# Kernel tuning notes

Measured on AMD Instinct MI355X. Metric: run time of the kernel, lower is better.

## Reference

```python
import jax, jax.numpy as jnp
import numpy as np

HIDDEN = 2048
NUM_HEADS = 32
NUM_KV_HEADS = 8
HEAD_DIM = HIDDEN // NUM_HEADS  # 64


def setup_inputs() -> dict:
    key = jax.random.key(0)
    ks = jax.random.split(key, 5)
    s = 0.02
    x = jax.random.normal(ks[0], (2, 2048, HIDDEN), dtype=jnp.float32)
    Wq = jax.random.normal(ks[1], (HIDDEN, NUM_HEADS * HEAD_DIM), dtype=jnp.float32) * s
    Wk = jax.random.normal(ks[2], (HIDDEN, NUM_KV_HEADS * HEAD_DIM), dtype=jnp.float32) * s
    Wv = jax.random.normal(ks[3], (HIDDEN, NUM_KV_HEADS * HEAD_DIM), dtype=jnp.float32) * s
    Wo = jax.random.normal(ks[4], (NUM_HEADS * HEAD_DIM, HIDDEN), dtype=jnp.float32) * s
    return {"x": x, "Wq": Wq, "Wk": Wk, "Wv": Wv, "Wo": Wo}


def reference(x, Wq, Wk, Wv, Wo):
    b, s, _ = x.shape
    # projections: [b, s, h, d] -> [b, h, s, d]
    q = (x @ Wq).reshape(b, s, NUM_HEADS, HEAD_DIM).transpose(0, 2, 1, 3)
    k = (x @ Wk).reshape(b, s, NUM_KV_HEADS, HEAD_DIM).transpose(0, 2, 1, 3)
    v = (x @ Wv).reshape(b, s, NUM_KV_HEADS, HEAD_DIM).transpose(0, 2, 1, 3)
    rep = NUM_HEADS // NUM_KV_HEADS
    # repeat_interleave along head dim (consecutive copies), matching torch
    k = jnp.repeat(k, rep, axis=1)
    v = jnp.repeat(v, rep, axis=1)
    scale = HEAD_DIM ** (-0.5)
    attn = jnp.einsum("bhqd,bhkd->bhqk", q, k) * scale  # [b,h,s,s]
    attn = jax.nn.softmax(attn, axis=-1)
    out = jnp.einsum("bhqk,bhkd->bhqd", attn, v)
    out = out.transpose(0, 2, 1, 3).reshape(b, s, NUM_HEADS * HEAD_DIM)
    return out @ Wo
```

## Files before the change

### kernel.cpp

```cpp
#include <hip/hip_runtime.h>

typedef __attribute__((ext_vector_type(8))) short short8;
typedef __attribute__((ext_vector_type(4))) float f32x4;
typedef __attribute__((ext_vector_type(4))) unsigned short u16x4;
typedef __attribute__((ext_vector_type(8))) unsigned short u16x8;

__device__ __forceinline__ unsigned short f2bf(float f) {
  union { float f; unsigned u; } v; v.f = f;
  unsigned r = v.u + 0x7FFFu + ((v.u >> 16) & 1u);
  return (unsigned short)(r >> 16);
}

#define GLL16(g, l) \
  __builtin_amdgcn_global_load_lds((const __attribute__((address_space(1))) void*)(g), \
                                   (__attribute__((address_space(3))) void*)(l), 16, 0, 0)

__device__ __forceinline__ void tpose_body(const float* __restrict__ in,
                                           unsigned short* __restrict__ out,
                                           int C, int ldo, int c0, int r0,
                                           float (*tile)[33], int tx, int ty) {
#pragma unroll
  for (int i = 0; i < 4; ++i)
    tile[ty + i * 8][tx] = in[(size_t)(r0 + ty + i * 8) * C + c0 + tx];
  __syncthreads();
#pragma unroll
  for (int i = 0; i < 4; ++i)
    out[(size_t)(c0 + ty + i * 8) * ldo + r0 + tx] = f2bf(tile[tx][ty + i * 8]);
}

__global__ __launch_bounds__(256) void prep_kernel(const float* __restrict__ x,
                                                   const float* __restrict__ Wq,
                                                   const float* __restrict__ Wk,
                                                   const float* __restrict__ Wv,
                                                   const float* __restrict__ Wo,
                                                   unsigned short* __restrict__ xb,
                                                   unsigned short* __restrict__ wqkvt,
                                                   unsigned short* __restrict__ wot) {
  __shared__ float tile[32][33];
  const int bid = blockIdx.x;
  if (bid < 4096) {
    const int i = bid * 256 + threadIdx.x;
    const f32x4* p = (const f32x4*)x;
    f32x4 a = p[2 * i], b = p[2 * i + 1];
    u16x8 r;
    r[0] = f2bf(a[0]); r[1] = f2bf(a[1]); r[2] = f2bf(a[2]); r[3] = f2bf(a[3]);
    r[4] = f2bf(b[0]); r[5] = f2bf(b[1]); r[6] = f2bf(b[2]); r[7] = f2bf(b[3]);
    ((u16x8*)xb)[i] = r;
    return;
  }
  const int tx = threadIdx.x & 31, ty = threadIdx.x >> 5;
  int b2 = bid - 4096;
  if (b2 < 4096) {
    tpose_body(Wq, wqkvt, 2048, 2048, (b2 & 63) * 32, (b2 >> 6) * 32, tile, tx, ty);
    return;
  }
  b2 -= 4096;
  if (b2 < 1024) {
    tpose_body(Wk, wqkvt + (size_t)2048 * 2048, 512, 2048, (b2 & 15) * 32, (b2 >> 4) * 32, tile, tx, ty);
    return;
  }
  b2 -= 1024;
  if (b2 < 1024) {
    tpose_body(Wv, wqkvt + (size_t)2560 * 2048, 512, 2048, (b2 & 15) * 32, (b2 >> 4) * 32, tile, tx, ty);
    return;
  }
  b2 -= 1024;
  tpose_body(Wo, wot, 2048, 2048, (b2 & 63) * 32, (b2 >> 6) * 32, tile, tx, ty);
}

__global__ __launch_bounds__(256) void gemm_qkv_kernel(const unsigned short* __restrict__ A,
                                                       const unsigned short* __restrict__ BT,
                                                       unsigned short* __restrict__ Cq,
                                                       unsigned short* __restrict__ VT) {
  __shared__ unsigned short As[2][128 * 32];
  __shared__ unsigned short Bs[2][128 * 32];
  const int tid = threadIdx.x;
  const int wave = tid >> 6, lane = tid & 63;
  const int r16 = lane & 15, g = lane >> 4;
  const int n0 = blockIdx.x * 128, m0 = blockIdx.y * 128;
  const int wr = wave >> 1, wc = wave & 1;
  f32x4 acc[4][4] = {};
  const int so = wave * 1024 + lane * 16;

  auto STAGE = [&](int kt, int bufi) {
    const int k0 = kt * 32;
#pragma unroll
    for (int i = 0; i < 2; ++i) {
      const int o = i * 4096 + so;
      const int row = o >> 6;
      const int ke = (o & 63) >> 1;
      GLL16(A + (size_t)(m0 + row) * 2048 + k0 + ke, (char*)As[bufi] + i * 4096 + wave * 1024);
      GLL16(BT + (size_t)(n0 + row) * 2048 + k0 + ke, (char*)Bs[bufi] + i * 4096 + wave * 1024);
    }
  };
  STAGE(0, 0);
  __syncthreads();
  for (int kt = 0; kt < 64; ++kt) {
    const int cur = kt & 1;
    if (kt < 63) STAGE(kt + 1, cur ^ 1);
    short8 af[4], bfr[4];
#pragma unroll
    for (int mi = 0; mi < 4; ++mi) {
      const int row = wr * 64 + mi * 16 + r16;
      af[mi] = *(const short8*)((const char*)As[cur] + row * 64 + g * 16);
    }
#pragma unroll
    for (int ni = 0; ni < 4; ++ni) {
      const int row = wc * 64 + ni * 16 + r16;
      bfr[ni] = *(const short8*)((const char*)Bs[cur] + row * 64 + g * 16);
    }
#pragma unroll
    for (int mi = 0; mi < 4; ++mi)
#pragma unroll
      for (int ni = 0; ni < 4; ++ni)
        acc[mi][ni] = __builtin_amdgcn_mfma_f32_16x16x32_bf16(af[mi], bfr[ni], acc[mi][ni], 0, 0, 0);
    __syncthreads();
  }
  const float qs = 0.18033688f;
#pragma unroll
  for (int mi = 0; mi < 4; ++mi) {
#pragma unroll
    for (int ni = 0; ni < 4; ++ni) {
      const int n = n0 + wc * 64 + ni * 16 + r16;
      const int mb = m0 + wr * 64 + mi * 16 + g * 4;
      f32x4 v = acc[mi][ni];
      if (n < 2560) {
        const float s = (n < 2048) ? qs : 1.0f;
#pragma unroll
        for (int r = 0; r < 4; ++r) Cq[(size_t)(mb + r) * 3072 + n] = f2bf(v[r] * s);
      } else {
        const int d = n - 2560;
        const int bb = mb >> 11, s0 = mb & 2047;
        const int s0p = (s0 & ~31) | (((s0 >> 2) & 3) << 3) | (((s0 >> 4) & 1) << 2);
        u16x4 pk;
#pragma unroll
        for (int r = 0; r < 4; ++r) pk[r] = f2bf(v[r]);
        *(u16x4*)(VT + (size_t)(bb * 512 + d) * 2048 + s0p) = pk;
      }
    }
  }
}

__global__ __launch_bounds__(256) void gemm_out_kernel(const unsigned short* __restrict__ A,
                                                       const unsigned short* __restrict__ BT,
                                                       float* __restrict__ Co) {
  __shared__ unsigned short As[2][128 * 32];
  __shared__ unsigned short Bs[2][128 * 32];
  const int tid = threadIdx.x;
  const int wave = tid >> 6, lane = tid & 63;
  const int r16 = lane & 15, g = lane >> 4;
  const int n0 = blockIdx.x * 128, m0 = blockIdx.y * 128;
  const int wr = wave >> 1, wc = wave & 1;
  f32x4 acc[4][4] = {};
  const int so = wave * 1024 + lane * 16;

  auto STAGE = [&](int kt, int bufi) {
    const int k0 = kt * 32;
#pragma unroll
    for (int i = 0; i < 2; ++i) {
      const int o = i * 4096 + so;
      const int row = o >> 6;
      const int ke = (o & 63) >> 1;
      GLL16(A + (size_t)(m0 + row) * 2048 + k0 + ke, (char*)As[bufi] + i * 4096 + wave * 1024);
      GLL16(BT + (size_t)(n0 + row) * 2048 + k0 + ke, (char*)Bs[bufi] + i * 4096 + wave * 1024);
    }
  };
  STAGE(0, 0);
  __syncthreads();
  for (int kt = 0; kt < 64; ++kt) {
    const int cur = kt & 1;
    if (kt < 63) STAGE(kt + 1, cur ^ 1);
    short8 af[4], bfr[4];
#pragma unroll
    for (int mi = 0; mi < 4; ++mi) {
      const int row = wr * 64 + mi * 16 + r16;
      af[mi] = *(const short8*)((const char*)As[cur] + row * 64 + g * 16);
    }
#pragma unroll
    for (int ni = 0; ni < 4; ++ni) {
      const int row = wc * 64 + ni * 16 + r16;
      bfr[ni] = *(const short8*)((const char*)Bs[cur] + row * 64 + g * 16);
    }
#pragma unroll
    for (int mi = 0; mi < 4; ++mi)
#pragma unroll
      for (int ni = 0; ni < 4; ++ni)
        acc[mi][ni] = __builtin_amdgcn_mfma_f32_16x16x32_bf16(af[mi], bfr[ni], acc[mi][ni], 0, 0, 0);
    __syncthreads();
  }
#pragma unroll
  for (int mi = 0; mi < 4; ++mi)
#pragma unroll
    for (int ni = 0; ni < 4; ++ni) {
      const int n = n0 + wc * 64 + ni * 16 + r16;
      const int mb = m0 + wr * 64 + mi * 16 + g * 4;
      f32x4 v = acc[mi][ni];
#pragma unroll
      for (int r = 0; r < 4; ++r) Co[(size_t)(mb + r) * 2048 + n] = v[r];
    }
}

__global__ __launch_bounds__(512) void attn_kernel(const unsigned short* __restrict__ QKV,
                                                   const unsigned short* __restrict__ VT,
                                                   unsigned short* __restrict__ O) {
  __shared__ unsigned short Ks[2][64 * 64];
  __shared__ unsigned short Vs[2][64 * 64];
  const int tid = threadIdx.x;
  const int wave = tid >> 6, lane = tid & 63;
  const int r16 = lane & 15, g = lane >> 4;
  const int qt = blockIdx.x, bh = blockIdx.y;
  const int b = bh >> 5, h = bh & 31, kvh = h >> 2;
  const int qtok0 = b * 2048 + qt * 128 + wave * 16;
  short8 qf[2];
#pragma unroll
  for (int kh = 0; kh < 2; ++kh)
    qf[kh] = *(const short8*)(QKV + (size_t)(qtok0 + r16) * 3072 + h * 64 + kh * 32 + g * 8);
  union { unsigned u[4]; short8 s; } ones;
  ones.u[0] = ones.u[1] = ones.u[2] = ones.u[3] = 0x3F803F80u;
  f32x4 oa[4] = {};
  f32x4 lacc = {};
  const unsigned short* Kb = QKV + (size_t)b * 2048 * 3072 + 2048 + kvh * 64;
  const unsigned short* Vb = VT + (size_t)(b * 512 + kvh * 64) * 2048;
  const int so = wave * 1024 + lane * 16;

  auto STAGE = [&](int t, int bufi) {
    const int kv0 = t * 64;
    const int row = so >> 7;
    const int c = ((((so >> 4) & 7) ^ (row & 7))) * 8;
    GLL16(Kb + (size_t)(kv0 + row) * 3072 + c, (char*)Ks[bufi] + wave * 1024);
    GLL16(Vb + (size_t)row * 2048 + kv0 + c, (char*)Vs[bufi] + wave * 1024);
  };
  STAGE(0, 0);
  __syncthreads();
  for (int t = 0; t < 32; ++t) {
    const int cur = t & 1;
    if (t < 31) STAGE(t + 1, cur ^ 1);
    f32x4 sc[4];
    __builtin_amdgcn_s_setprio(1);
#pragma unroll
    for (int jt = 0; jt < 4; ++jt) {
      const int j = jt * 16 + r16;
      short8 kf0 = *(const short8*)((const char*)Ks[cur] + j * 128 + ((g * 16) ^ ((j & 7) << 4)));
      short8 kf1 = *(const short8*)((const char*)Ks[cur] + j * 128 + ((64 + g * 16) ^ ((j & 7) << 4)));
      f32x4 z = {-8.f, -8.f, -8.f, -8.f};
      z = __builtin_amdgcn_mfma_f32_16x16x32_bf16(kf0, qf[0], z, 0, 0, 0);
      z = __builtin_amdgcn_mfma_f32_16x16x32_bf16(kf1, qf[1], z, 0, 0, 0);
      sc[jt] = z;
    }
    __builtin_amdgcn_s_setprio(0);
    short8 pa[2];
    {
      unsigned pk[4][2];
#pragma unroll
      for (int jt = 0; jt < 4; ++jt) {
        float p0 = __builtin_amdgcn_exp2f(sc[jt][0]);
        float p1 = __builtin_amdgcn_exp2f(sc[jt][1]);
        float p2 = __builtin_amdgcn_exp2f(sc[jt][2]);
        float p3 = __builtin_amdgcn_exp2f(sc[jt][3]);
        asm("v_cvt_pk_bf16_f32 %0, %1, %2" : "=v"(pk[jt][0]) : "v"(p0), "v"(p1));
        asm("v_cvt_pk_bf16_f32 %0, %1, %2" : "=v"(pk[jt][1]) : "v"(p2), "v"(p3));
      }
#pragma unroll
      for (int kh = 0; kh < 2; ++kh) {
        union { unsigned u[4]; short8 s; } pu;
        pu.u[0] = pk[2 * kh][0]; pu.u[1] = pk[2 * kh][1];
        pu.u[2] = pk[2 * kh + 1][0]; pu.u[3] = pk[2 * kh + 1][1];
        pa[kh] = pu.s;
      }
    }
    __builtin_amdgcn_s_setprio(1);
    lacc = __builtin_amdgcn_mfma_f32_16x16x32_bf16(pa[0], ones.s, lacc, 0, 0, 0);
    lacc = __builtin_amdgcn_mfma_f32_16x16x32_bf16(pa[1], ones.s, lacc, 0, 0, 0);
#pragma unroll
    for (int dt = 0; dt < 4; ++dt) {
      const int d = dt * 16 + r16;
      const char* vrow = (const char*)Vs[cur] + d * 128;
      const int sw = (d & 7) << 4;
#pragma unroll
      for (int kh = 0; kh < 2; ++kh) {
        short8 vf = *(const short8*)(vrow + ((kh * 64 + g * 16) ^ sw));
        oa[dt] = __builtin_amdgcn_mfma_f32_16x16x32_bf16(pa[kh], vf, oa[dt], 0, 0, 0);
      }
    }
    __builtin_amdgcn_s_setprio(0);
    __syncthreads();
  }
#pragma unroll
  for (int dt = 0; dt < 4; ++dt)
#pragma unroll
    for (int r = 0; r < 4; ++r)
      O[(size_t)(qtok0 + g * 4 + r) * 2048 + h * 64 + dt * 16 + r16] =
          f2bf(oa[dt][r] / lacc[r]);
}

extern "C" void kernel_launch(void* const* d_in, const int* in_sizes, int n_in,
                              void* d_out, int out_size, void* d_ws, size_t ws_size,
                              hipStream_t stream) {
  const float* x  = (const float*)d_in[0];
  const float* Wq = (const float*)d_in[1];
  const float* Wk = (const float*)d_in[2];
  const float* Wv = (const float*)d_in[3];
  const float* Wo = (const float*)d_in[4];
  char* w = (char*)d_ws;
  unsigned short* xb    = (unsigned short*)(w);
  unsigned short* wqkvt = (unsigned short*)(w + 16777216);
  unsigned short* wot   = (unsigned short*)(w + 29360128);
  unsigned short* qkv   = (unsigned short*)(w + 37748736);
  unsigned short* vt    = (unsigned short*)(w + 62914560);
  unsigned short* ob    = (unsigned short*)(w + 67108864);
  float* out = (float*)d_out;

  prep_kernel<<<14336, 256, 0, stream>>>(x, Wq, Wk, Wv, Wo, xb, wqkvt, wot);
  gemm_qkv_kernel<<<dim3(24, 32), 256, 0, stream>>>(xb, wqkvt, qkv, vt);
  attn_kernel<<<dim3(16, 64), 512, 0, stream>>>(qkv, vt, ob);
  gemm_out_kernel<<<dim3(16, 32), 256, 0, stream>>>(ob, wot, out);
}
```

Measured before the change: 237.7 us.

## Triple-buffer K/V tiles and software-pipeline QK of next tile with PV

Moves the attention loop from double to triple buffering of the K/V shared-memory tiles, staging two tiles ahead. It computes the QK scores for tile t+1 before the softmax and PV of tile t, so the MFMA work of one tile overlaps the exp and convert work of the other, and it hoists the V fragment loads ahead of the exp block. It also adds a minimum-occupancy hint of 4 to the launch bounds. The cost is more LDS and more live registers, which could cap occupancy or cause spills.

```diff
diff --git a/kernel.cpp b/kernel.cpp
--- a/kernel.cpp
+++ b/kernel.cpp
@@ -200,11 +200,11 @@
     }
 }
 
-__global__ __launch_bounds__(512) void attn_kernel(const unsigned short* __restrict__ QKV,
-                                                   const unsigned short* __restrict__ VT,
-                                                   unsigned short* __restrict__ O) {
-  __shared__ unsigned short Ks[2][64 * 64];
-  __shared__ unsigned short Vs[2][64 * 64];
+__global__ __launch_bounds__(512, 4) void attn_kernel(const unsigned short* __restrict__ QKV,
+                                                      const unsigned short* __restrict__ VT,
+                                                      unsigned short* __restrict__ O) {
+  __shared__ unsigned short Ks[3][64 * 64];
+  __shared__ unsigned short Vs[3][64 * 64];
   const int tid = threadIdx.x;
   const int wave = tid >> 6, lane = tid & 63;
   const int r16 = lane & 15, g = lane >> 4;
@@ -222,32 +222,39 @@
   const unsigned short* Kb = QKV + (size_t)b * 2048 * 3072 + 2048 + kvh * 64;
   const unsigned short* Vb = VT + (size_t)(b * 512 + kvh * 64) * 2048;
   const int so = wave * 1024 + lane * 16;
-
-  auto STAGE = [&](int t, int bufi) {
+  const int srow = so >> 7;
+  const int scol = ((((so >> 4) & 7) ^ (srow & 7))) * 8;
+
+  auto STAGE = [&](int t, unsigned short* kd, unsigned short* vd) {
     const int kv0 = t * 64;
-    const int row = so >> 7;
-    const int c = ((((so >> 4) & 7) ^ (row & 7))) * 8;
-    GLL16(Kb + (size_t)(kv0 + row) * 3072 + c, (char*)Ks[bufi] + wave * 1024);
-    GLL16(Vb + (size_t)row * 2048 + kv0 + c, (char*)Vs[bufi] + wave * 1024);
-  };
-  STAGE(0, 0);
-  __syncthreads();
-  for (int t = 0; t < 32; ++t) {
-    const int cur = t & 1;
-    if (t < 31) STAGE(t + 1, cur ^ 1);
-    f32x4 sc[4];
+    GLL16(Kb + (size_t)(kv0 + srow) * 3072 + scol, (char*)kd + wave * 1024);
+    GLL16(Vb + (size_t)srow * 2048 + kv0 + scol, (char*)vd + wave * 1024);
+  };
+  auto QK = [&](const unsigned short* kbuf, f32x4 (&sc)[4]) {
     __builtin_amdgcn_s_setprio(1);
 #pragma unroll
     for (int jt = 0; jt < 4; ++jt) {
       const int j = jt * 16 + r16;
-      short8 kf0 = *(const short8*)((const char*)Ks[cur] + j * 128 + ((g * 16) ^ ((j & 7) << 4)));
-      short8 kf1 = *(const short8*)((const char*)Ks[cur] + j * 128 + ((64 + g * 16) ^ ((j & 7) << 4)));
+      short8 kf0 = *(const short8*)((const char*)kbuf + j * 128 + ((g * 16) ^ ((j & 7) << 4)));
+      short8 kf1 = *(const short8*)((const char*)kbuf + j * 128 + ((64 + g * 16) ^ ((j & 7) << 4)));
       f32x4 z = {-8.f, -8.f, -8.f, -8.f};
       z = __builtin_amdgcn_mfma_f32_16x16x32_bf16(kf0, qf[0], z, 0, 0, 0);
       z = __builtin_amdgcn_mfma_f32_16x16x32_bf16(kf1, qf[1], z, 0, 0, 0);
       sc[jt] = z;
     }
     __builtin_amdgcn_s_setprio(0);
+  };
+  auto SMPV = [&](const f32x4 (&sc)[4], const unsigned short* vbuf) {
+    short8 vf[4][2];
+#pragma unroll
+    for (int dt = 0; dt < 4; ++dt) {
+      const int d = dt * 16 + r16;
+      const char* vrow = (const char*)vbuf + d * 128;
+      const int sw = (d & 7) << 4;
+#pragma unroll
+      for (int kh = 0; kh < 2; ++kh)
+        vf[dt][kh] = *(const short8*)(vrow + ((kh * 64 + g * 16) ^ sw));
+    }
     short8 pa[2];
     {
       unsigned pk[4][2];
@@ -272,18 +279,33 @@
     lacc = __builtin_amdgcn_mfma_f32_16x16x32_bf16(pa[0], ones.s, lacc, 0, 0, 0);
     lacc = __builtin_amdgcn_mfma_f32_16x16x32_bf16(pa[1], ones.s, lacc, 0, 0, 0);
 #pragma unroll
-    for (int dt = 0; dt < 4; ++dt) {
-      const int d = dt * 16 + r16;
-      const char* vrow = (const char*)Vs[cur] + d * 128;
-      const int sw = (d & 7) << 4;
-#pragma unroll
-      for (int kh = 0; kh < 2; ++kh) {
-        short8 vf = *(const short8*)(vrow + ((kh * 64 + g * 16) ^ sw));
-        oa[dt] = __builtin_amdgcn_mfma_f32_16x16x32_bf16(pa[kh], vf, oa[dt], 0, 0, 0);
-      }
-    }
+    for (int dt = 0; dt < 4; ++dt)
+#pragma unroll
+      for (int kh = 0; kh < 2; ++kh)
+        oa[dt] = __builtin_amdgcn_mfma_f32_16x16x32_bf16(pa[kh], vf[dt][kh], oa[dt], 0, 0, 0);
     __builtin_amdgcn_s_setprio(0);
+  };
+
+  unsigned short *cK = Ks[0], *nK = Ks[1], *sK = Ks[2];
+  unsigned short *cV = Vs[0], *nV = Vs[1], *sV = Vs[2];
+  STAGE(0, cK, cV);
+  STAGE(1, nK, nV);
+  __syncthreads();
+  f32x4 scA[4], scB[4];
+  QK(cK, scA);
+  STAGE(2, sK, sV);
+
+  auto step = [&](const f32x4 (&scC)[4], f32x4 (&scN)[4], int t) {
+    if (t + 1 < 32) QK(nK, scN);
+    SMPV(scC, cV);
     __syncthreads();
+    if (t + 3 < 32) STAGE(t + 3, cK, cV);
+    unsigned short* tk = cK; cK = nK; nK = sK; sK = tk;
+    unsigned short* tv = cV; cV = nV; nV = sV; sV = tv;
+  };
+  for (int tt = 0; tt < 16; ++tt) {
+    step(scA, scB, 2 * tt);
+    step(scB, scA, 2 * tt + 1);
   }
 #pragma unroll
   for (int dt = 0; dt < 4; ++dt)
```

New measurement: 229.6 us. -3.4%, faster.
